# Performance work log

Hardware: AMD Instinct MI355X
Metric: run time of the kernel (lower is better)

The kernel has to match this reference:

```python
import jax, jax.numpy as jnp
import numpy as np

EPS = 1e-5
NEIGHBOR_K = 3
NEG_SLOPE = 0.2

def _conv(x, w):
    # x: [N,C,H,W], w: [O,I,3,3], stride 1, SAME padding
    return jax.lax.conv_general_dilated(
        x, w, window_strides=(1, 1), padding='SAME',
        dimension_numbers=('NCHW', 'OIHW', 'NCHW'))

def _bn(x, gamma, beta):
    # BatchNorm2d in training mode: batch statistics over (N,H,W), biased var
    m = x.mean(axis=(0, 2, 3), keepdims=True)
    v = x.var(axis=(0, 2, 3), keepdims=True)
    xn = (x - m) * jax.lax.rsqrt(v + EPS)
    return xn * gamma.reshape(1, -1, 1, 1) + beta.reshape(1, -1, 1, 1)

def _lrelu(x):
    return jnp.where(x >= 0, x, NEG_SLOPE * x)

def _maxpool2(x):
    return jax.lax.reduce_window(x, -jnp.inf, jax.lax.max,
                                 (1, 1, 2, 2), (1, 1, 2, 2), 'VALID')

def _features(x, w1, g1, b1, w2, g2, b2, w3, g3, b3, w4, g4, b4):
    x = _maxpool2(_lrelu(_bn(_conv(x, w1), g1, b1)))
    x = _maxpool2(_lrelu(_bn(_conv(x, w2), g2, b2)))
    x = _lrelu(_bn(_conv(x, w3), g3, b3))
    x = _lrelu(_bn(_conv(x, w4), g4, b4))
    return x  # [N, 64, 21, 21]

def setup_inputs() -> dict:
    key = jax.random.key(0)
    ks = jax.random.split(key, 8)
    inp = {
        'input1': jax.random.normal(ks[0], (32, 3, 84, 84), jnp.float32),
        'input2': jax.random.normal(ks[1], (5, 5, 3, 84, 84), jnp.float32),
        'w1': jax.random.normal(ks[2], (64, 3, 3, 3), jnp.float32) * 0.1,
        'g1': jax.random.uniform(ks[3], (64,), jnp.float32, 0.5, 1.5),
        'b1': jnp.zeros((64,), jnp.float32),
        'w2': jax.random.normal(ks[4], (64, 64, 3, 3), jnp.float32) * 0.1,
        'g2': jax.random.uniform(ks[5], (64,), jnp.float32, 0.5, 1.5),
        'b2': jnp.zeros((64,), jnp.float32),
        'w3': jax.random.normal(ks[6], (64, 64, 3, 3), jnp.float32) * 0.1,
        'g3': jax.random.uniform(ks[7], (64,), jnp.float32, 0.5, 1.5),
        'b3': jnp.zeros((64,), jnp.float32),
        'w4': jax.random.normal(jax.random.fold_in(key, 100), (64, 64, 3, 3), jnp.float32) * 0.1,
        'g4': jax.random.uniform(jax.random.fold_in(key, 101), (64,), jnp.float32, 0.5, 1.5),
        'b4': jnp.zeros((64,), jnp.float32),
    }
    return inp

def reference(input1, input2, w1, g1, b1, w2, g2, b2, w3, g3, b3, w4, g4, b4):
    params = (w1, g1, b1, w2, g2, b2, w3, g3, b3, w4, g4, b4)
    # Query features: [B, C, h, w]
    q = _features(input1, *params)
    B, C, h, w = q.shape
    hw = h * w
    Q = q.reshape(B, C, hw).transpose(0, 2, 1)            # [B, hw, C]
    qn = jnp.linalg.norm(Q, axis=2, keepdims=True)        # [B, hw, 1]
    # Support features, BN stats per class-batch (matches per-class forward)
    s = jax.vmap(lambda x: _features(x, *params))(input2) # [nc, shot, C, h, w]
    nc, shot = s.shape[0], s.shape[1]
    S = s.transpose(0, 2, 1, 3, 4).reshape(nc, C, shot * hw)  # [nc, C, M]
    sn = jnp.linalg.norm(S, axis=1, keepdims=True)            # [nc, 1, M]
    # Cosine similarities: [B, nc, hw, M]
    sims = jnp.einsum('bqc,ncm->bnqm', Q, S)
    sims = sims / (qn[:, None, :, :] * sn[None, :, :, :])
    topv = jax.lax.top_k(sims, NEIGHBOR_K)[0]              # [B, nc, hw, k]
    return topv.sum(axis=(2, 3))                           # [B, nc]
```

## Files before the change

kernel.cpp:

```cpp
#include <hip/hip_runtime.h>
#include <hip/hip_bf16.h>
#include <stdint.h>

#define NQ 32
#define NCLS 5
#define SHOT 5
#define NIMG 57
#define P1 7056
#define P2 1764
#define P3 441
#define MM (SHOT*P3)
#define EPSB 1e-5f
#define SLOPE 0.2f
#define NEGINF -3.4e38f
#define NREP 32
#define MCH 18

typedef __attribute__((ext_vector_type(8))) short short8;
typedef __attribute__((ext_vector_type(4))) float f32x4;

__device__ inline float ldf(const float* p) { return *p; }
__device__ inline float ldf(const __hip_bfloat16* p) { return __bfloat162float(*p); }

__device__ __forceinline__ unsigned short bf16bits(float v)
{
    __hip_bfloat16 h = __float2bfloat16(v);
    return *reinterpret_cast<unsigned short*>(&h);
}

__global__ void pack_all_k(const float* __restrict__ w1, const float* __restrict__ w2,
                           const float* __restrict__ w3, const float* __restrict__ w4,
                           unsigned short* __restrict__ wpk1, unsigned short* __restrict__ wpk2,
                           unsigned short* __restrict__ wpk3, unsigned short* __restrict__ wpk4)
{
    int i = blockIdx.x * 256 + threadIdx.x;
    if (i < 3 * 36864) {
        int set = i / 36864, ii = i - set * 36864;
        const float* w = (set == 0) ? w2 : (set == 1) ? w3 : w4;
        unsigned short* wpk = (set == 0) ? wpk2 : (set == 1) ? wpk3 : wpk4;
        int j = ii & 7, lane = (ii >> 3) & 63, chunk = ii >> 9;
        int nt = chunk & 3, half = (chunk >> 2) & 1, t = chunk >> 3;
        int co = nt * 16 + (lane & 15);
        int ci = half * 32 + (lane >> 4) * 8 + j;
        wpk[ii] = bf16bits(w[co * 576 + ci * 9 + t]);
    } else {
        int ii = i - 3 * 36864;
        if (ii >= 4096) return;
        int j = ii & 7, lane = (ii >> 3) & 63, c8 = ii >> 9;
        int nt = c8 & 3, f = c8 >> 2;
        int co = nt * 16 + (lane & 15), q = lane >> 4;
        int k = q * 8 + j;
        float val = 0.f;
        if (f == 0) {
            int t = k >> 2, ci = k & 3;
            if (ci < 3) val = w1[co * 27 + ci * 9 + t];
        } else if (k < 4) {
            int ci = k & 3;
            if (ci < 3) val = w1[co * 27 + ci * 9 + 8];
        }
        wpk1[ii] = bf16bits(val);
    }
}

__global__ __launch_bounds__(256) void conv1m_k(const float* __restrict__ in1,
                                                const float* __restrict__ in2,
                                                const unsigned short* __restrict__ wpk1,
                                                __hip_bfloat16* __restrict__ out,
                                                float* __restrict__ sums)
{
    constexpr int S = 84, P = P1, MBLK = 256, NB = 28, SPAN = MBLK + 2 * S + 2;
    __shared__ __align__(16) unsigned short ls4[SPAN * 4];
    __shared__ float qs[4][64], qs2[4][64];
    int img = blockIdx.x / NB;
    int p0 = (blockIdx.x % NB) * MBLK;
    int tid = threadIdx.x, lane = tid & 63, wv = tid >> 6;
    int col = lane & 15, quad = lane >> 4;
    const float* in = (img < NQ) ? in1 + (size_t)img * 3 * P1
                                 : in2 + (size_t)(img - NQ) * 3 * P1;
    for (int u = tid; u < SPAN; u += 256) {
        int p = p0 - S - 1 + u;
        union { unsigned short us[4]; uint2 u2; } o;
        o.u2 = (uint2){0u, 0u};
        if (p >= 0 && p < P) {
            o.us[0] = bf16bits(in[p]);
            o.us[1] = bf16bits(in[P1 + p]);
            o.us[2] = bf16bits(in[2 * P1 + p]);
        }
        *(uint2*)(ls4 + u * 4) = o.u2;
    }
    const short8* wb = (const short8*)wpk1;
    short8 b0[4], b1[4];
    #pragma unroll
    for (int nt = 0; nt < 4; ++nt) {
        b0[nt] = wb[(size_t)(nt * 64 + lane)];
        b1[nt] = wb[(size_t)((4 + nt) * 64 + lane)];
    }
    int t0 = 2 * quad, t1 = t0 + 1;
    int d0 = (t0 / 3 - 1) * S + (t0 % 3 - 1);
    int d1 = (t1 / 3 - 1) * S + (t1 % 3 - 1);
    const int d8 = S + 1;
    int tx0 = t0 % 3, tx1 = t1 % 3;
    __syncthreads();
    f32x4 acc[4][4];
    #pragma unroll
    for (int mt = 0; mt < 4; ++mt)
        #pragma unroll
        for (int nt = 0; nt < 4; ++nt) acc[mt][nt] = (f32x4){0.f, 0.f, 0.f, 0.f};
    #pragma unroll
    for (int mt = 0; mt < 4; ++mt) {
        int pl = wv * 64 + mt * 16 + col;
        int xm = (p0 + pl) % S;
        int base = pl + S + 1;
        uint2 h0 = *(const uint2*)(ls4 + (base + d0) * 4);
        uint2 h1 = *(const uint2*)(ls4 + (base + d1) * 4);
        uint2 h8 = *(const uint2*)(ls4 + (base + d8) * 4);
        bool ok0 = (tx0 == 0) ? (xm >= 1) : ((tx0 == 2) ? (xm <= S - 2) : true);
        bool ok1 = (tx1 == 0) ? (xm >= 1) : ((tx1 == 2) ? (xm <= S - 2) : true);
        bool ok8 = (quad == 0) && (xm <= S - 2);
        if (!ok0) h0 = (uint2){0u, 0u};
        if (!ok1) h1 = (uint2){0u, 0u};
        if (!ok8) h8 = (uint2){0u, 0u};
        union { uint4 u; short8 s; } ca, cb;
        ca.u = (uint4){h0.x, h0.y, h1.x, h1.y};
        cb.u = (uint4){h8.x, h8.y, 0u, 0u};
        #pragma unroll
        for (int nt = 0; nt < 4; ++nt) {
            acc[mt][nt] = __builtin_amdgcn_mfma_f32_16x16x32_bf16(ca.s, b0[nt], acc[mt][nt], 0, 0, 0);
            acc[mt][nt] = __builtin_amdgcn_mfma_f32_16x16x32_bf16(cb.s, b1[nt], acc[mt][nt], 0, 0, 0);
        }
    }
    float s[4] = {0.f, 0.f, 0.f, 0.f}, s2[4] = {0.f, 0.f, 0.f, 0.f};
    __hip_bfloat16* ob = out + (size_t)img * P * 64;
    #pragma unroll
    for (int mt = 0; mt < 4; ++mt) {
        int tb = p0 + wv * 64 + mt * 16 + quad * 4;
        #pragma unroll
        for (int reg = 0; reg < 4; ++reg) {
            int pr = tb + reg;
            if (pr < P) {
                #pragma unroll
                for (int nt = 0; nt < 4; ++nt) {
                    float v = acc[mt][nt][reg];
                    ob[(size_t)pr * 64 + nt * 16 + col] = __float2bfloat16(v);
                    s[nt] += v;
                    s2[nt] = fmaf(v, v, s2[nt]);
                }
            }
        }
    }
    #pragma unroll
    for (int d = 16; d < 64; d <<= 1)
        #pragma unroll
        for (int nt = 0; nt < 4; ++nt) {
            s[nt] += __shfl_xor(s[nt], d, 64);
            s2[nt] += __shfl_xor(s2[nt], d, 64);
        }
    if (quad == 0) {
        #pragma unroll
        for (int nt = 0; nt < 4; ++nt) {
            qs[wv][nt * 16 + col] = s[nt];
            qs2[wv][nt * 16 + col] = s2[nt];
        }
    }
    __syncthreads();
    if (wv == 0) {
        int g = (img < NQ) ? 0 : 1 + (img - NQ) / SHOT;
        int rep = blockIdx.x & (NREP - 1);
        float ts = qs[0][lane] + qs[1][lane] + qs[2][lane] + qs[3][lane];
        float ts2 = qs2[0][lane] + qs2[1][lane] + qs2[2][lane] + qs2[3][lane];
        float* base = sums + ((size_t)(g * 64 + lane) * 2) * NREP + rep;
        atomicAdd(base, ts);
        atomicAdd(base + NREP, ts2);
    }
}

template <int S, int MBLK>
__global__ __launch_bounds__(256) void conv64m_k(const unsigned short* __restrict__ in,
                                                 const unsigned short* __restrict__ wpk,
                                                 float* __restrict__ out,
                                                 float* __restrict__ sums)
{
    constexpr int P = S * S;
    constexpr int MT = MBLK / 64;
    constexpr int NB = (P + MBLK - 1) / MBLK;
    constexpr int SPAN = MBLK + 2 * S + 2;
    __shared__ __align__(16) unsigned short ls[SPAN * 72];
    __shared__ float qs[4][64], qs2[4][64];
    int img = blockIdx.x / NB;
    int p0 = (blockIdx.x % NB) * MBLK;
    int tid = threadIdx.x;
    int lane = tid & 63, wv = tid >> 6;
    int col = lane & 15, quad = lane >> 4;
    const unsigned short* ib = in + (size_t)img * P * 64;
    for (int u = tid; u < SPAN * 8; u += 256) {
        int pix = u >> 3, part = u & 7;
        int p = p0 - S - 1 + pix;
        short8 v = {0, 0, 0, 0, 0, 0, 0, 0};
        if (p >= 0 && p < P) v = *(const short8*)(ib + (size_t)p * 64 + part * 8);
        *(short8*)(ls + pix * 72 + part * 8) = v;
    }
    __syncthreads();
    f32x4 acc[MT][4];
    #pragma unroll
    for (int mt = 0; mt < MT; ++mt)
        #pragma unroll
        for (int nt = 0; nt < 4; ++nt) acc[mt][nt] = (f32x4){0.f, 0.f, 0.f, 0.f};
    bool mok0[MT], mok2[MT];
    #pragma unroll
    for (int mt = 0; mt < MT; ++mt) {
        int xm = (p0 + wv * (MT * 16) + mt * 16 + col) % S;
        mok0[mt] = xm >= 1;
        mok2[mt] = xm <= S - 2;
    }
    const short8* wb = (const short8*)wpk;
    #pragma unroll
    for (int ky = 0; ky < 3; ++ky) {
        #pragma unroll
        for (int kx = 0; kx < 3; ++kx) {
            int t = ky * 3 + kx;
            int d = (ky - 1) * S + (kx - 1);
            #pragma unroll
            for (int half = 0; half < 2; ++half) {
                short8 b[4];
                #pragma unroll
                for (int nt = 0; nt < 4; ++nt)
                    b[nt] = wb[((t * 2 + half) * 4 + nt) * 64 + lane];
                #pragma unroll
                for (int mt = 0; mt < MT; ++mt) {
                    int idx = wv * (MT * 16) + mt * 16 + col + S + 1 + d;
                    short8 a = *(const short8*)(ls + idx * 72 + half * 32 + quad * 8);
                    bool ok = (kx == 0) ? mok0[mt] : (kx == 2) ? mok2[mt] : true;
                    if (!ok) a = (short8){0, 0, 0, 0, 0, 0, 0, 0};
                    #pragma unroll
                    for (int nt = 0; nt < 4; ++nt)
                        acc[mt][nt] = __builtin_amdgcn_mfma_f32_16x16x32_bf16(a, b[nt], acc[mt][nt], 0, 0, 0);
                }
            }
        }
    }
    float s[4] = {0.f, 0.f, 0.f, 0.f}, s2[4] = {0.f, 0.f, 0.f, 0.f};
    float* ob = out + (size_t)img * P * 64;
    #pragma unroll
    for (int mt = 0; mt < MT; ++mt) {
        int tb = p0 + wv * (MT * 16) + mt * 16 + quad * 4;
        #pragma unroll
        for (int reg = 0; reg < 4; ++reg) {
            int pr = tb + reg;
            if (pr < P) {
                #pragma unroll
                for (int nt = 0; nt < 4; ++nt) {
                    float v = acc[mt][nt][reg];
                    ob[(size_t)pr * 64 + nt * 16 + col] = v;
                    s[nt] += v;
                    s2[nt] = fmaf(v, v, s2[nt]);
                }
            }
        }
    }
    #pragma unroll
    for (int d = 16; d < 64; d <<= 1)
        #pragma unroll
        for (int nt = 0; nt < 4; ++nt) {
            s[nt] += __shfl_xor(s[nt], d, 64);
            s2[nt] += __shfl_xor(s2[nt], d, 64);
        }
    if (quad == 0) {
        #pragma unroll
        for (int nt = 0; nt < 4; ++nt) {
            qs[wv][nt * 16 + col] = s[nt];
            qs2[wv][nt * 16 + col] = s2[nt];
        }
    }
    __syncthreads();
    if (wv == 0) {
        int g = (img < NQ) ? 0 : 1 + (img - NQ) / SHOT;
        int rep = blockIdx.x & (NREP - 1);
        float ts = qs[0][lane] + qs[1][lane] + qs[2][lane] + qs[3][lane];
        float ts2 = qs2[0][lane] + qs2[1][lane] + qs2[2][lane] + qs2[3][lane];
        float* base = sums + ((size_t)(g * 64 + lane) * 2) * NREP + rep;
        atomicAdd(base, ts);
        atomicAdd(base + NREP, ts2);
    }
}

__global__ void finalize_k(const float* __restrict__ sums, float* __restrict__ ms,
                           const float* __restrict__ gamma, const float* __restrict__ beta, int P)
{
    int i = blockIdx.x * blockDim.x + threadIdx.x;
    if (i >= 6 * 64) return;
    int g = i >> 6, c = i & 63;
    const float* ps = sums + (size_t)i * 2 * NREP;
    float s = 0.f, s2 = 0.f;
    #pragma unroll
    for (int r = 0; r < NREP; ++r) { s += ps[r]; s2 += ps[NREP + r]; }
    float cnt = (float)((g == 0 ? NQ : SHOT) * P);
    float mean = s / cnt;
    float var = s2 / cnt - mean * mean;
    float a = rsqrtf(var + EPSB) * gamma[c];
    ms[i * 2] = a;
    ms[i * 2 + 1] = fmaf(-mean, a, beta[c]);
}

template <typename T>
__global__ __launch_bounds__(256) void bnpool_k(const T* __restrict__ x, const float* __restrict__ ms,
                                                __hip_bfloat16* __restrict__ out, int Win)
{
    int Wout = Win >> 1, Pout = Wout * Wout;
    size_t idx = (size_t)blockIdx.x * 256 + threadIdx.x;
    size_t total = (size_t)NIMG * Pout * 64;
    if (idx >= total) return;
    int c = (int)(idx & 63);
    size_t t = idx >> 6;
    int p = (int)(t % Pout);
    int img = (int)(t / Pout);
    int y = p / Wout, xo = p - y * Wout;
    int g = (img < NQ) ? 0 : 1 + (img - NQ) / SHOT;
    float a = ms[(g * 64 + c) * 2], bb = ms[(g * 64 + c) * 2 + 1];
    const T* base = x + (((size_t)img * Win + 2 * y) * Win + 2 * xo) * 64 + c;
    float mx = -3.4e38f;
    #pragma unroll
    for (int dy = 0; dy < 2; ++dy)
        #pragma unroll
        for (int dx = 0; dx < 2; ++dx) {
            float v = ldf(base + ((size_t)dy * Win + dx) * 64);
            v = fmaf(v, a, bb);
            v = v >= 0.f ? v : SLOPE * v;
            mx = fmaxf(mx, v);
        }
    out[idx] = __float2bfloat16(mx);
}

__global__ __launch_bounds__(256) void bnact_k(const float* __restrict__ x, const float* __restrict__ ms,
                                               __hip_bfloat16* __restrict__ out)
{
    size_t idx = (size_t)blockIdx.x * 256 + threadIdx.x;
    size_t total = (size_t)NIMG * P3 * 64;
    if (idx >= total) return;
    int c = (int)(idx & 63);
    int img = (int)(idx >> 6) / P3;
    int g = (img < NQ) ? 0 : 1 + (img - NQ) / SHOT;
    float v = fmaf(x[idx], ms[(g * 64 + c) * 2], ms[(g * 64 + c) * 2 + 1]);
    out[idx] = __float2bfloat16(v >= 0.f ? v : SLOPE * v);
}

__global__ __launch_bounds__(256) void bnnorm_k(const float* __restrict__ x, const float* __restrict__ ms,
                                                __hip_bfloat16* __restrict__ out)
{
    int lane = threadIdx.x & 63, wvr = threadIdx.x >> 6;
    int pix = blockIdx.x * 4 + wvr;
    if (pix >= NIMG * P3) return;
    int img = pix / P3;
    int g = (img < NQ) ? 0 : 1 + (img - NQ) / SHOT;
    float v = fmaf(x[(size_t)pix * 64 + lane], ms[(g * 64 + lane) * 2], ms[(g * 64 + lane) * 2 + 1]);
    v = v >= 0.f ? v : SLOPE * v;
    float ss = v * v;
    #pragma unroll
    for (int d = 32; d > 0; d >>= 1) ss += __shfl_xor(ss, d, 64);
    out[(size_t)pix * 64 + lane] = __float2bfloat16(v * rsqrtf(ss));
}

__device__ __forceinline__ void ins3(float v, float& t0, float& t1, float& t2)
{
    float n1 = __builtin_amdgcn_fmed3f(v, t0, t1);
    float n2 = __builtin_amdgcn_fmed3f(v, t1, t2);
    t0 = fmaxf(t0, v);
    t1 = n1;
    t2 = n2;
}

__global__ __launch_bounds__(256) void sim_k(const __hip_bfloat16* __restrict__ fhat,
                                             float* __restrict__ out)
{
    __shared__ __align__(16) unsigned short sl[2][128 * 72];
    int t = blockIdx.x;
    int qb = t % 7;
    int n = (t / 7) % NCLS;
    int bq = t / (7 * NCLS);
    int tid = threadIdx.x, lane = tid & 63, wv = tid >> 6;
    int col = lane & 15, quad = lane >> 4;
    int q = qb * 64 + wv * 16 + col;
    int qc = q < P3 ? q : P3 - 1;
    const unsigned short* qp = (const unsigned short*)fhat + ((size_t)bq * P3 + qc) * 64;
    short8 a0 = *(const short8*)(qp + quad * 8);
    short8 a1 = *(const short8*)(qp + 32 + quad * 8);
    const unsigned short* sp = (const unsigned short*)fhat + (size_t)(NQ + n * SHOT) * P3 * 64;
    int srow = tid >> 3;
    int scc = (tid & 7) * 8;
    const short8 z8 = {0, 0, 0, 0, 0, 0, 0, 0};
    float t0[4], t1[4], t2[4];
    #pragma unroll
    for (int i = 0; i < 4; ++i) { t0[i] = NEGINF; t1[i] = NEGINF; t2[i] = NEGINF; }
    short8 r[4];
    #pragma unroll
    for (int i = 0; i < 4; ++i) {
        int m = srow + i * 32;
        r[i] = (m < MM) ? *(const short8*)(sp + (size_t)m * 64 + scc) : z8;
    }
    #pragma unroll
    for (int i = 0; i < 4; ++i)
        *(short8*)(&sl[0][(srow + i * 32) * 72 + scc]) = r[i];
    __syncthreads();
    for (int c = 0; c < MCH; ++c) {
        int m0 = c * 128;
        if (c + 1 < MCH) {
            int mb = m0 + 128;
            #pragma unroll
            for (int i = 0; i < 4; ++i) {
                int m = mb + srow + i * 32;
                r[i] = (m < MM) ? *(const short8*)(sp + (size_t)m * 64 + scc) : z8;
            }
        }
        const unsigned short* sb = sl[c & 1];
        #pragma unroll
        for (int mt = 0; mt < 8; ++mt) {
            int mbase = m0 + mt * 16;
            if (mbase < MM) {
                const unsigned short* sr = sb + (mt * 16 + col) * 72;
                short8 b0 = *(const short8*)(sr + quad * 8);
                short8 b1 = *(const short8*)(sr + 32 + quad * 8);
                f32x4 acc = {0.f, 0.f, 0.f, 0.f};
                acc = __builtin_amdgcn_mfma_f32_16x16x32_bf16(a0, b0, acc, 0, 0, 0);
                acc = __builtin_amdgcn_mfma_f32_16x16x32_bf16(a1, b1, acc, 0, 0, 0);
                if (mbase + 15 < MM) {
                    #pragma unroll
                    for (int i = 0; i < 4; ++i) ins3(acc[i], t0[i], t1[i], t2[i]);
                } else {
                    float bias = (mbase + col < MM) ? 0.f : NEGINF;
                    #pragma unroll
                    for (int i = 0; i < 4; ++i) ins3(acc[i] + bias, t0[i], t1[i], t2[i]);
                }
            }
        }
        if (c + 1 < MCH) {
            #pragma unroll
            for (int i = 0; i < 4; ++i)
                *(short8*)(&sl[(c + 1) & 1][(srow + i * 32) * 72 + scc]) = r[i];
        }
        __syncthreads();
    }
    #pragma unroll
    for (int d = 1; d < 16; d <<= 1) {
        #pragma unroll
        for (int i = 0; i < 4; ++i) {
            float u0 = __shfl_xor(t0[i], d, 64);
            float u1 = __shfl_xor(t1[i], d, 64);
            float u2 = __shfl_xor(t2[i], d, 64);
            ins3(u0, t0[i], t1[i], t2[i]);
            ins3(u1, t0[i], t1[i], t2[i]);
            ins3(u2, t0[i], t1[i], t2[i]);
        }
    }
    if (col == 0) {
        float s = 0.f;
        int q0 = qb * 64 + wv * 16 + quad * 4;
        #pragma unroll
        for (int i = 0; i < 4; ++i)
            if (q0 + i < P3) s += t0[i] + t1[i] + t2[i];
        atomicAdd(&out[bq * NCLS + n], s);
    }
}

extern "C" void kernel_launch(void* const* d_in, const int* in_sizes, int n_in,
                              void* d_out, int out_size, void* d_ws, size_t ws_size,
                              hipStream_t stream)
{
    const float* input1 = (const float*)d_in[0];
    const float* input2 = (const float*)d_in[1];
    const float* w1 = (const float*)d_in[2];
    const float* g1 = (const float*)d_in[3];
    const float* b1 = (const float*)d_in[4];
    const float* w2 = (const float*)d_in[5];
    const float* g2 = (const float*)d_in[6];
    const float* b2 = (const float*)d_in[7];
    const float* w3 = (const float*)d_in[8];
    const float* g3 = (const float*)d_in[9];
    const float* b3 = (const float*)d_in[10];
    const float* w4 = (const float*)d_in[11];
    const float* g4 = (const float*)d_in[12];
    const float* b4 = (const float*)d_in[13];
    float* out = (float*)d_out;

    char* w8 = (char*)d_ws;
    const size_t oB = 51480576;
    const size_t oT = oB + 12870144;
    const size_t STG = 6 * 64 * 2 * NREP * sizeof(float);
    __hip_bfloat16* conv1raw = (__hip_bfloat16*)(w8 + 0);
    float* conv2raw = (float*)(w8 + 0);
    float* conv3raw = (float*)(w8 + 0);
    __hip_bfloat16* act3 = (__hip_bfloat16*)(w8 + 6435072);
    float* conv4raw = (float*)(w8 + 9652608);
    __hip_bfloat16* fhat = (__hip_bfloat16*)(w8 + 16087680);
    __hip_bfloat16* pooled1 = (__hip_bfloat16*)(w8 + oB);
    __hip_bfloat16* pooled2 = (__hip_bfloat16*)(w8 + oB);
    float* sums = (float*)(w8 + oT);
    float* ms = (float*)(w8 + oT + 4 * STG);
    unsigned short* wpk2 = (unsigned short*)(w8 + oT + 4 * STG + 12288);
    unsigned short* wpk3 = (unsigned short*)(w8 + oT + 4 * STG + 12288 + 73728);
    unsigned short* wpk4 = (unsigned short*)(w8 + oT + 4 * STG + 12288 + 147456);
    unsigned short* wpk1 = (unsigned short*)(w8 + oT + 4 * STG + 12288 + 221184);
    if (ws_size < oT + 4 * STG + 12288 + 221184 + 8192) return;
    float* sums1 = sums;
    float* sums2 = sums + 6 * 64 * 2 * NREP;
    float* sums3 = sums2 + 6 * 64 * 2 * NREP;
    float* sums4 = sums3 + 6 * 64 * 2 * NREP;

    hipMemsetAsync(d_out, 0, (size_t)out_size * sizeof(float), stream);
    hipMemsetAsync(sums, 0, 4 * STG, stream);

    pack_all_k<<<448, 256, 0, stream>>>(w1, w2, w3, w4, wpk1, wpk2, wpk3, wpk4);

    conv1m_k<<<NIMG * 28, 256, 0, stream>>>(input1, input2, wpk1, conv1raw, sums1);
    finalize_k<<<2, 256, 0, stream>>>(sums1, ms + 0, g1, b1, P1);
    bnpool_k<__hip_bfloat16><<<25137, 256, 0, stream>>>(conv1raw, ms + 0, pooled1, 84);
    conv64m_k<42, 256><<<NIMG * 7, 256, 0, stream>>>((const unsigned short*)pooled1, wpk2, conv2raw, sums2);
    finalize_k<<<2, 256, 0, stream>>>(sums2, ms + 768, g2, b2, P2);
    bnpool_k<float><<<6285, 256, 0, stream>>>(conv2raw, ms + 768, pooled2, 42);
    conv64m_k<21, 128><<<NIMG * 4, 256, 0, stream>>>((const unsigned short*)pooled2, wpk3, conv3raw, sums3);
    finalize_k<<<2, 256, 0, stream>>>(sums3, ms + 1536, g3, b3, P3);
    bnact_k<<<6285, 256, 0, stream>>>(conv3raw, ms + 1536, act3);
    conv64m_k<21, 128><<<NIMG * 4, 256, 0, stream>>>((const unsigned short*)act3, wpk4, conv4raw, sums4);
    finalize_k<<<2, 256, 0, stream>>>(sums4, ms + 2304, g4, b4, P3);
    bnnorm_k<<<6285, 256, 0, stream>>>(conv4raw, ms + 2304, fhat);
    sim_k<<<NQ * NCLS * 7, 256, 0, stream>>>(fhat, out);
}
```

Before: 262.1 us.

## Split support tiles across waves with per-wave query tiles and LDS top-3 merge

The similarity kernel now has each wave process all 64 queries of the block (four 16-row query tiles held in registers) over its own quarter of the support rows. Support fragments are loaded directly from global memory with register prefetching, so the shared-memory staging and per-chunk barriers go away. Each wave's per-query top-3 is merged across waves through a small LDS buffer, and one atomic is issued per block. This removes LDS traffic and synchronisation and reuses each support fragment across four MFMA query tiles. In exchange it raises register pressure with 48 top-k accumulators per lane and relies on uncoalesced direct global loads.

```diff
diff --git a/kernel.cpp b/kernel.cpp
--- a/kernel.cpp
+++ b/kernel.cpp
@@ -14,7 +14,7 @@
 #define SLOPE 0.2f
 #define NEGINF -3.4e38f
 #define NREP 32
-#define MCH 18
+#define MTILES 138
 
 typedef __attribute__((ext_vector_type(8))) short short8;
 typedef __attribute__((ext_vector_type(4))) float f32x4;
@@ -371,92 +371,106 @@
 __global__ __launch_bounds__(256) void sim_k(const __hip_bfloat16* __restrict__ fhat,
                                              float* __restrict__ out)
 {
-    __shared__ __align__(16) unsigned short sl[2][128 * 72];
+    __shared__ float mg[3][4][64];
     int t = blockIdx.x;
     int qb = t % 7;
     int n = (t / 7) % NCLS;
     int bq = t / (7 * NCLS);
     int tid = threadIdx.x, lane = tid & 63, wv = tid >> 6;
     int col = lane & 15, quad = lane >> 4;
-    int q = qb * 64 + wv * 16 + col;
-    int qc = q < P3 ? q : P3 - 1;
-    const unsigned short* qp = (const unsigned short*)fhat + ((size_t)bq * P3 + qc) * 64;
-    short8 a0 = *(const short8*)(qp + quad * 8);
-    short8 a1 = *(const short8*)(qp + 32 + quad * 8);
+    short8 a0[4], a1[4];
+    #pragma unroll
+    for (int qt = 0; qt < 4; ++qt) {
+        int q = qb * 64 + qt * 16 + col;
+        int qc = q < P3 ? q : P3 - 1;
+        const unsigned short* qp = (const unsigned short*)fhat + ((size_t)bq * P3 + qc) * 64;
+        a0[qt] = *(const short8*)(qp + quad * 8);
+        a1[qt] = *(const short8*)(qp + 32 + quad * 8);
+    }
     const unsigned short* sp = (const unsigned short*)fhat + (size_t)(NQ + n * SHOT) * P3 * 64;
-    int srow = tid >> 3;
-    int scc = (tid & 7) * 8;
-    const short8 z8 = {0, 0, 0, 0, 0, 0, 0, 0};
-    float t0[4], t1[4], t2[4];
-    #pragma unroll
-    for (int i = 0; i < 4; ++i) { t0[i] = NEGINF; t1[i] = NEGINF; t2[i] = NEGINF; }
-    short8 r[4];
-    #pragma unroll
-    for (int i = 0; i < 4; ++i) {
-        int m = srow + i * 32;
-        r[i] = (m < MM) ? *(const short8*)(sp + (size_t)m * 64 + scc) : z8;
-    }
-    #pragma unroll
-    for (int i = 0; i < 4; ++i)
-        *(short8*)(&sl[0][(srow + i * 32) * 72 + scc]) = r[i];
+    int tb = wv * 36;
+    int te = tb + 36 < MTILES ? tb + 36 : MTILES;
+    float t0[4][4], t1[4][4], t2[4][4];
+    #pragma unroll
+    for (int qt = 0; qt < 4; ++qt)
+        #pragma unroll
+        for (int r = 0; r < 4; ++r) { t0[qt][r] = NEGINF; t1[qt][r] = NEGINF; t2[qt][r] = NEGINF; }
+    short8 nb0, nb1;
+    {
+        int row = tb * 16 + col;
+        row = row < MM ? row : MM - 1;
+        const unsigned short* p = sp + (size_t)row * 64 + quad * 8;
+        nb0 = *(const short8*)p;
+        nb1 = *(const short8*)(p + 32);
+    }
+    for (int mt = tb; mt < te; ++mt) {
+        short8 b0 = nb0, b1 = nb1;
+        if (mt + 1 < te) {
+            int row = (mt + 1) * 16 + col;
+            row = row < MM ? row : MM - 1;
+            const unsigned short* p = sp + (size_t)row * 64 + quad * 8;
+            nb0 = *(const short8*)p;
+            nb1 = *(const short8*)(p + 32);
+        }
+        if (mt * 16 + 15 < MM) {
+            #pragma unroll
+            for (int qt = 0; qt < 4; ++qt) {
+                f32x4 acc = {0.f, 0.f, 0.f, 0.f};
+                acc = __builtin_amdgcn_mfma_f32_16x16x32_bf16(a0[qt], b0, acc, 0, 0, 0);
+                acc = __builtin_amdgcn_mfma_f32_16x16x32_bf16(a1[qt], b1, acc, 0, 0, 0);
+                #pragma unroll
+                for (int r = 0; r < 4; ++r) ins3(acc[r], t0[qt][r], t1[qt][r], t2[qt][r]);
+            }
+        } else {
+            float bias = (mt * 16 + col < MM) ? 0.f : NEGINF;
+            #pragma unroll
+            for (int qt = 0; qt < 4; ++qt) {
+                f32x4 acc = {0.f, 0.f, 0.f, 0.f};
+                acc = __builtin_amdgcn_mfma_f32_16x16x32_bf16(a0[qt], b0, acc, 0, 0, 0);
+                acc = __builtin_amdgcn_mfma_f32_16x16x32_bf16(a1[qt], b1, acc, 0, 0, 0);
+                #pragma unroll
+                for (int r = 0; r < 4; ++r) ins3(acc[r] + bias, t0[qt][r], t1[qt][r], t2[qt][r]);
+            }
+        }
+    }
+    #pragma unroll
+    for (int d = 1; d < 16; d <<= 1)
+        #pragma unroll
+        for (int qt = 0; qt < 4; ++qt)
+            #pragma unroll
+            for (int r = 0; r < 4; ++r) {
+                float u0 = __shfl_xor(t0[qt][r], d, 64);
+                float u1 = __shfl_xor(t1[qt][r], d, 64);
+                float u2 = __shfl_xor(t2[qt][r], d, 64);
+                ins3(u0, t0[qt][r], t1[qt][r], t2[qt][r]);
+                ins3(u1, t0[qt][r], t1[qt][r], t2[qt][r]);
+                ins3(u2, t0[qt][r], t1[qt][r], t2[qt][r]);
+            }
+    if (col == 0) {
+        #pragma unroll
+        for (int qt = 0; qt < 4; ++qt)
+            #pragma unroll
+            for (int r = 0; r < 4; ++r) {
+                int ql = qt * 16 + quad * 4 + r;
+                mg[0][wv][ql] = t0[qt][r];
+                mg[1][wv][ql] = t1[qt][r];
+                mg[2][wv][ql] = t2[qt][r];
+            }
+    }
     __syncthreads();
-    for (int c = 0; c < MCH; ++c) {
-        int m0 = c * 128;
-        if (c + 1 < MCH) {
-            int mb = m0 + 128;
-            #pragma unroll
-            for (int i = 0; i < 4; ++i) {
-                int m = mb + srow + i * 32;
-                r[i] = (m < MM) ? *(const short8*)(sp + (size_t)m * 64 + scc) : z8;
-            }
-        }
-        const unsigned short* sb = sl[c & 1];
-        #pragma unroll
-        for (int mt = 0; mt < 8; ++mt) {
-            int mbase = m0 + mt * 16;
-            if (mbase < MM) {
-                const unsigned short* sr = sb + (mt * 16 + col) * 72;
-                short8 b0 = *(const short8*)(sr + quad * 8);
-                short8 b1 = *(const short8*)(sr + 32 + quad * 8);
-                f32x4 acc = {0.f, 0.f, 0.f, 0.f};
-                acc = __builtin_amdgcn_mfma_f32_16x16x32_bf16(a0, b0, acc, 0, 0, 0);
-                acc = __builtin_amdgcn_mfma_f32_16x16x32_bf16(a1, b1, acc, 0, 0, 0);
-                if (mbase + 15 < MM) {
-                    #pragma unroll
-                    for (int i = 0; i < 4; ++i) ins3(acc[i], t0[i], t1[i], t2[i]);
-                } else {
-                    float bias = (mbase + col < MM) ? 0.f : NEGINF;
-                    #pragma unroll
-                    for (int i = 0; i < 4; ++i) ins3(acc[i] + bias, t0[i], t1[i], t2[i]);
-                }
-            }
-        }
-        if (c + 1 < MCH) {
-            #pragma unroll
-            for (int i = 0; i < 4; ++i)
-                *(short8*)(&sl[(c + 1) & 1][(srow + i * 32) * 72 + scc]) = r[i];
-        }
-        __syncthreads();
-    }
-    #pragma unroll
-    for (int d = 1; d < 16; d <<= 1) {
-        #pragma unroll
-        for (int i = 0; i < 4; ++i) {
-            float u0 = __shfl_xor(t0[i], d, 64);
-            float u1 = __shfl_xor(t1[i], d, 64);
-            float u2 = __shfl_xor(t2[i], d, 64);
-            ins3(u0, t0[i], t1[i], t2[i]);
-            ins3(u1, t0[i], t1[i], t2[i]);
-            ins3(u2, t0[i], t1[i], t2[i]);
-        }
-    }
-    if (col == 0) {
-        float s = 0.f;
-        int q0 = qb * 64 + wv * 16 + quad * 4;
-        #pragma unroll
-        for (int i = 0; i < 4; ++i)
-            if (q0 + i < P3) s += t0[i] + t1[i] + t2[i];
-        atomicAdd(&out[bq * NCLS + n], s);
+    if (wv == 0) {
+        float v0 = mg[0][0][lane], v1 = mg[1][0][lane], v2 = mg[2][0][lane];
+        #pragma unroll
+        for (int w = 1; w < 4; ++w) {
+            ins3(mg[0][w][lane], v0, v1, v2);
+            ins3(mg[1][w][lane], v0, v1, v2);
+            ins3(mg[2][w][lane], v0, v1, v2);
+        }
+        float s = v0 + v1 + v2;
+        if (qb * 64 + lane >= P3) s = 0.f;
+        #pragma unroll
+        for (int d = 32; d > 0; d >>= 1) s += __shfl_xor(s, d, 64);
+        if (lane == 0) atomicAdd(&out[bq * NCLS + n], s);
     }
 }
 
```

After: 268.1 us. 1.02x slower.
